# Kernel optimization log

Hardware: AMD Instinct MI355X
Metric: run time of the kernel (lower is better)

## Reference

```python
import jax, jax.numpy as jnp
import numpy as np

N, D_IN, D_P, N_HEADS, N_CTRS, D_OUT = 8192, 256, 64, 8, 128, 256


def setup_inputs() -> dict:
    key = jax.random.key(0)
    k = jax.random.split(key, 6)
    x = jax.random.normal(k[0], (N, D_IN), dtype=jnp.float32)
    ctrs = jax.random.normal(k[1], (N_HEADS, N_CTRS, D_P), dtype=jnp.float32) * 0.5
    Wv = jax.random.normal(k[2], (N_HEADS, N_CTRS, D_P, D_P), dtype=jnp.float32) * 0.02
    Ov = jax.random.normal(k[3], (N_HEADS, N_CTRS, D_P), dtype=jnp.float32) * 0.02
    Wq = jax.random.normal(k[4], (D_IN, D_P, N_HEADS), dtype=jnp.float32) * 0.05
    Wo = jax.random.normal(k[5], (N_HEADS * D_P, D_OUT), dtype=jnp.float32) * 0.02
    return {"x": x, "ctrs": ctrs, "Wv": Wv, "Ov": Ov, "Wq": Wq, "Wo": Wo}


def reference(x, ctrs, Wv, Ov, Wq, Wo):
    # project input per head: (N,d_in) x (d_in,d_p,h) -> (h,N,d_p)
    x_in = jnp.einsum('ni,iph->hnp', x, Wq)
    # RBF soft assignments over centroids: (h,N,c)
    dist_sq = jnp.sum((x_in[:, :, None, :] - ctrs[:, None, :, :]) ** 2, axis=-1)
    assignments = jax.nn.softmax(-dist_sq, axis=2)
    # soft-weighted per-cluster matrices: (h,N,g,p)
    scored_weights = jnp.einsum('hnc,hcgp->hngp', assignments, Wv)
    # soft-weighted offsets: (h,N,p)
    scored_offsets = jnp.einsum('hnc,hcp->hnp', assignments, Ov)
    # elementwise multiply (broadcast over g) then reduce over g, as in original
    heads_out = jnp.sum(scored_weights * x_in[:, :, None, :], axis=2) + scored_offsets
    # NOTE: original reshapes (h,N,p) directly into (N, h*p) in row-major order
    heads_out = heads_out.reshape(x.shape[0], N_HEADS * D_P)
    return heads_out @ Wo
```

## Files before the change

### kernel.cpp

```cpp
#include <hip/hip_runtime.h>
#include <math.h>

#define NROWS 8192
#define DIN   256
#define NH    8
#define NC    128
#define DOUT  256

typedef unsigned short ushort_t;
typedef __attribute__((ext_vector_type(8))) short bf16x8;
typedef __attribute__((ext_vector_type(4))) float f32x4;
typedef __attribute__((ext_vector_type(8))) unsigned short u16x8;

static __device__ __forceinline__ ushort_t f2bf(float f) {
  union { float f; unsigned u; } v; v.f = f;
  unsigned r = v.u + 0x7fffu + ((v.u >> 16) & 1u);
  return (ushort_t)(r >> 16);
}
static __device__ __forceinline__ float bf2f(ushort_t h) {
  union { unsigned u; float f; } v; v.u = ((unsigned)h) << 16;
  return v.f;
}

#define MFMA16(a, b, c) __builtin_amdgcn_mfma_f32_16x16x32_bf16((a), (b), (c), 0, 0, 0)
#define GLOAD_LDS16(g, l)                                                     \
  __builtin_amdgcn_global_load_lds(                                           \
      (const __attribute__((address_space(1))) void*)(g),                     \
      (__attribute__((address_space(3))) void*)(l), 16, 0, 0)

__global__ __launch_bounds__(256) void prep_kernel(
    const float* __restrict__ Wq, const float* __restrict__ ctrs,
    const float* __restrict__ Wo, const float* __restrict__ Wv,
    const float* __restrict__ Ov, ushort_t* __restrict__ wcvtT,
    ushort_t* __restrict__ ctr3T, float* __restrict__ cbias,
    ushort_t* __restrict__ WoT, ushort_t* __restrict__ W2bT) {
  int bid = blockIdx.x;
  int t = threadIdx.x;
  if (bid < 512) {
    int j = bid, k = t;
    int h = j >> 6, p = j & 63;
    float v = Wq[((size_t)k * 64 + p) * 8 + h];
    ushort_t hi = f2bf(v), lo = f2bf(v - bf2f(hi));
    wcvtT[(size_t)j * 512 + k]       = hi;
    wcvtT[(size_t)j * 512 + 256 + k] = lo;
  } else if (bid < 768) {
    int idx = (bid - 512) * 4 + (t >> 6);
    int p = t & 63;
    float v = ctrs[(size_t)idx * 64 + p];
    float sq = v * v;
    #pragma unroll
    for (int off = 32; off >= 1; off >>= 1) sq += __shfl_xor(sq, off, 64);
    if (p == 0) cbias[idx] = -sq;
    ushort_t hi = f2bf(v), lo = f2bf(v - bf2f(hi));
    ctr3T[(size_t)idx * 192 + p]       = hi;
    ctr3T[(size_t)idx * 192 + 64 + p]  = lo;
    ctr3T[(size_t)idx * 192 + 128 + p] = hi;
  } else if (bid < 1280) {
    int k = bid - 768;
    int n = t;
    WoT[(size_t)n * 512 + k] = f2bf(Wo[(size_t)k * 256 + n]);
  } else {
    int b = (bid - 1280) * 4 + (t >> 6);
    int p = t & 63;
    int h = b >> 7, c = b & 127;
    const float* wv = Wv + (size_t)b * 4096;
    float acc = 0.f;
    #pragma unroll 16
    for (int g = 0; g < 64; ++g) acc += wv[g * 64 + p];
    W2bT[((size_t)h * 128 + p) * 128 + c]      = f2bf(acc);
    W2bT[((size_t)h * 128 + 64 + p) * 128 + c] = f2bf(Ov[(size_t)b * 64 + p]);
  }
}

__global__ __launch_bounds__(256) void gemm2_kernel(
    const ushort_t* __restrict__ A, const ushort_t* __restrict__ Bt,
    float* __restrict__ out) {
  __shared__ ushort_t At[32 * 64];
  __shared__ ushort_t Bl[64 * 64];
  const int t = threadIdx.x;
  const int w = t >> 6, l = t & 63;
  const int wr = w >> 1, wc = w & 1;
  const int m0 = (blockIdx.x >> 2) * 32, n0 = (blockIdx.x & 3) * 64;
  const int lr = l & 15, lk = l >> 4;

  f32x4 acc[2];
  #pragma unroll
  for (int b = 0; b < 2; ++b) acc[b] = (f32x4){0.f, 0.f, 0.f, 0.f};

  for (int k0 = 0; k0 < 512; k0 += 64) {
    {
      int q = w * 64 + l;
      int row = q >> 3, s = q & 7;
      int kl = k0 + ((s ^ (row & 7)) << 3);
      GLOAD_LDS16(A + (size_t)(m0 + row) * 512 + kl,
                  (char*)At + (size_t)w * 1024);
    }
    #pragma unroll
    for (int i = 0; i < 2; ++i) {
      int q = (i * 4 + w) * 64 + l;
      int row = q >> 3, s = q & 7;
      int kl = k0 + ((s ^ (row & 7)) << 3);
      GLOAD_LDS16(Bt + (size_t)(n0 + row) * 512 + kl,
                  (char*)Bl + (size_t)(i * 4 + w) * 1024);
    }
    __syncthreads();
    #pragma unroll
    for (int kk = 0; kk < 2; ++kk) {
      int rowa = wr * 16 + lr;
      int sa = (kk * 4 + lk) ^ (rowa & 7);
      bf16x8 af = *(const bf16x8*)((const char*)At + rowa * 128 + sa * 16);
      #pragma unroll
      for (int b = 0; b < 2; ++b) {
        int row = wc * 32 + b * 16 + lr;
        int s = (kk * 4 + lk) ^ (row & 7);
        bf16x8 bfr = *(const bf16x8*)((const char*)Bl + row * 128 + s * 16);
        acc[b] = MFMA16(af, bfr, acc[b]);
      }
    }
    __syncthreads();
  }
  #pragma unroll
  for (int b = 0; b < 2; ++b) {
    #pragma unroll
    for (int r = 0; r < 4; ++r) {
      int rowg = m0 + wr * 16 + lk * 4 + r;
      int colg = n0 + wc * 32 + b * 16 + lr;
      out[(size_t)rowg * 256 + colg] = acc[b][r];
    }
  }
}

__global__ __launch_bounds__(256, 2) void fused_pair_kernel(
    const float* __restrict__ x,
    const ushort_t* __restrict__ wcvtT,
    const ushort_t* __restrict__ ctr3T,
    const float* __restrict__ cbias,
    const ushort_t* __restrict__ W2bT,
    ushort_t* __restrict__ ho2) {
  __shared__ __align__(16) char Au_raw[36864];
  __shared__ char B0lds[16384];
  __shared__ char B1lds[16384];
  __shared__ float cb_lds[128];

  ushort_t* Axh = (ushort_t*)Au_raw;
  ushort_t* Axl = (ushort_t*)(Au_raw + 18432);
  ushort_t* A1  = (ushort_t*)Au_raw;
  ushort_t* A2  = (ushort_t*)Au_raw;

  const int t = threadIdx.x;
  const int w = t >> 6, l = t & 63;
  const int lr = l & 15, lk = l >> 4;
  const int h = blockIdx.x >> 6;
  const int n0 = (blockIdx.x & 63) * 128;

#define STAGE_B(BUF, SRC, LDB, KOFF)                                          \
  {                                                                           \
    _Pragma("unroll")                                                         \
    for (int i = 0; i < 4; ++i) {                                             \
      int q = (i * 4 + w) * 64 + l;                                           \
      int row = q >> 3, s = q & 7;                                            \
      GLOAD_LDS16((SRC) + (size_t)(h * 128 + row) * (LDB) + (KOFF) +          \
                      ((s ^ (row & 7)) << 3),                                 \
                  (char*)(BUF) + (size_t)(i * 4 + w) * 1024);                 \
    }                                                                         \
  }

#define STAGE_BX(BUF, KC)                                                     \
  {                                                                           \
    _Pragma("unroll")                                                         \
    for (int i = 0; i < 4; ++i) {                                             \
      int q = (i * 4 + w) * 64 + l;                                           \
      int row = q >> 3, s = q & 7;                                            \
      int sw = (s ^ (row & 7)) << 3;                                          \
      int jj = h * 64 + (row & 63);                                           \
      int koff = (row < 64 ? 0 : 256) + (KC) * 64 + sw;                       \
      GLOAD_LDS16(wcvtT + (size_t)jj * 512 + koff,                            \
                  (char*)(BUF) + (size_t)(i * 4 + w) * 1024);                 \
    }                                                                         \
  }

#define MFMA_STEP(BUF, ACC0, ACC1, KBASE, ASPLIT)                             \
  {                                                                           \
    _Pragma("unroll")                                                         \
    for (int kk = 0; kk < 2; ++kk) {                                          \
      int klog = (KBASE) + kk * 32 + lk * 8;                                  \
      int kp = (ASPLIT) ? (klog < 64 ? klog : klog - 64) : klog;              \
      bf16x8 af0 = *(const bf16x8*)&A1[(w * 16 + lr) * 136 + kp];             \
      bf16x8 af1 = *(const bf16x8*)&A1[(64 + w * 16 + lr) * 136 + kp];        \
      _Pragma("unroll")                                                       \
      for (int cj = 0; cj < 8; ++cj) {                                        \
        int brow = cj * 16 + lr;                                              \
        int slot = (kk * 4 + lk) ^ (brow & 7);                                \
        bf16x8 bfr =                                                          \
            *(const bf16x8*)((const char*)(BUF) + brow * 128 + slot * 16);    \
        (ACC0)[cj] = MFMA16(af0, bfr, (ACC0)[cj]);                            \
        (ACC1)[cj] = MFMA16(af1, bfr, (ACC1)[cj]);                            \
      }                                                                       \
    }                                                                         \
  }

#define MFMAX(BUF)                                                            \
  {                                                                           \
    _Pragma("unroll")                                                         \
    for (int kk = 0; kk < 2; ++kk) {                                          \
      bf16x8 ah0 = *(const bf16x8*)&Axh[(w * 16 + lr) * 72 + kk * 32 + lk * 8];     \
      bf16x8 al0 = *(const bf16x8*)&Axl[(w * 16 + lr) * 72 + kk * 32 + lk * 8];     \
      bf16x8 ah1 = *(const bf16x8*)&Axh[(64 + w * 16 + lr) * 72 + kk * 32 + lk * 8];\
      bf16x8 al1 = *(const bf16x8*)&Axl[(64 + w * 16 + lr) * 72 + kk * 32 + lk * 8];\
      _Pragma("unroll")                                                       \
      for (int cj = 0; cj < 4; ++cj) {                                        \
        int rh = cj * 16 + lr;                                                \
        int slot = (kk * 4 + lk) ^ (rh & 7);                                  \
        bf16x8 bh = *(const bf16x8*)((const char*)(BUF) + rh * 128 + slot * 16);\
        bf16x8 bl = *(const bf16x8*)((const char*)(BUF) + (64 + rh) * 128 + slot * 16);\
        acc_x0[cj] = MFMA16(ah0, bh, acc_x0[cj]);                             \
        acc_x0[cj] = MFMA16(al0, bh, acc_x0[cj]);                             \
        acc_x0[cj] = MFMA16(ah0, bl, acc_x0[cj]);                             \
        acc_x1[cj] = MFMA16(ah1, bh, acc_x1[cj]);                             \
        acc_x1[cj] = MFMA16(al1, bh, acc_x1[cj]);                             \
        acc_x1[cj] = MFMA16(ah1, bl, acc_x1[cj]);                             \
      }                                                                       \
    }                                                                         \
  }

#define BAR() __builtin_amdgcn_s_barrier()
#define SCHED() __builtin_amdgcn_sched_barrier(0)
#define WAITALL_BAR()                                                         \
  {                                                                           \
    asm volatile("s_waitcnt vmcnt(0) lgkmcnt(0)" ::: "memory");               \
    SCHED(); BAR(); SCHED();                                                  \
  }

  const int xrow = t >> 2;
  const int xseg = (t & 3) << 4;
  const float* xb0 = x + (size_t)(n0 + xrow) * 256 + xseg;
  const float* xb1 = xb0 + 64 * 256;
  float4 xr[8];

#define LOAD_X(KC)                                                            \
  {                                                                           \
    _Pragma("unroll")                                                         \
    for (int j = 0; j < 4; ++j) xr[j]     = *(const float4*)(xb0 + (KC) * 64 + j * 4); \
    _Pragma("unroll")                                                         \
    for (int j = 0; j < 4; ++j) xr[4 + j] = *(const float4*)(xb1 + (KC) * 64 + j * 4); \
  }

#define CVT_AX()                                                              \
  {                                                                           \
    _Pragma("unroll")                                                         \
    for (int hf = 0; hf < 2; ++hf) {                                          \
      u16x8 hv0, hv1, lv0, lv1;                                               \
      _Pragma("unroll")                                                       \
      for (int j = 0; j < 2; ++j) {                                           \
        float f4[8] = {xr[hf*4 + j*2].x, xr[hf*4 + j*2].y, xr[hf*4 + j*2].z,  \
                       xr[hf*4 + j*2].w, xr[hf*4 + j*2 + 1].x,                \
                       xr[hf*4 + j*2 + 1].y, xr[hf*4 + j*2 + 1].z,            \
                       xr[hf*4 + j*2 + 1].w};                                 \
        _Pragma("unroll")                                                     \
        for (int e = 0; e < 8; ++e) {                                         \
          ushort_t hi = f2bf(f4[e]);                                          \
          if (j == 0) { hv0[e] = hi; lv0[e] = f2bf(f4[e] - bf2f(hi)); }       \
          else        { hv1[e] = hi; lv1[e] = f2bf(f4[e] - bf2f(hi)); }       \
        }                                                                     \
      }                                                                       \
      int ro = hf * 64 + xrow;                                                \
      *(u16x8*)&Axh[ro * 72 + xseg]     = hv0;                                \
      *(u16x8*)&Axh[ro * 72 + xseg + 8] = hv1;                                \
      *(u16x8*)&Axl[ro * 72 + xseg]     = lv0;                                \
      *(u16x8*)&Axl[ro * 72 + xseg + 8] = lv1;                                \
    }                                                                         \
  }

#define SOFTMAX(ACC, ROFF)                                                    \
  {                                                                           \
    float cbv[8];                                                             \
    _Pragma("unroll")                                                         \
    for (int cj = 0; cj < 8; ++cj) cbv[cj] = cb_lds[cj * 16 + lr];            \
    _Pragma("unroll")                                                         \
    for (int r = 0; r < 4; ++r) {                                             \
      float v[8];                                                             \
      float m = -1e30f;                                                       \
      _Pragma("unroll")                                                       \
      for (int cj = 0; cj < 8; ++cj) {                                        \
        v[cj] = 2.f * (ACC)[cj][r] + cbv[cj];                                 \
        m = fmaxf(m, v[cj]);                                                  \
      }                                                                       \
      m = fmaxf(m, __shfl_xor(m, 1, 64));                                     \
      m = fmaxf(m, __shfl_xor(m, 2, 64));                                     \
      m = fmaxf(m, __shfl_xor(m, 4, 64));                                     \
      m = fmaxf(m, __shfl_xor(m, 8, 64));                                     \
      float s = 0.f;                                                          \
      _Pragma("unroll")                                                       \
      for (int cj = 0; cj < 8; ++cj) {                                        \
        v[cj] = __expf(v[cj] - m);                                            \
        s += v[cj];                                                           \
      }                                                                       \
      s += __shfl_xor(s, 1, 64);                                              \
      s += __shfl_xor(s, 2, 64);                                              \
      s += __shfl_xor(s, 4, 64);                                              \
      s += __shfl_xor(s, 8, 64);                                              \
      float inv = 1.f / s;                                                    \
      int row = (ROFF) + w * 16 + lk * 4 + r;                                 \
      _Pragma("unroll")                                                       \
      for (int cj = 0; cj < 8; ++cj)                                          \
        A2[row * 136 + cj * 16 + lr] = f2bf(v[cj] * inv);                     \
    }                                                                         \
  }

  cb_lds[t & 127] = cbias[h * 128 + (t & 127)];
  STAGE_BX(B0lds, 0);
  LOAD_X(0);
  f32x4 acc_x0[4], acc_x1[4];
  #pragma unroll
  for (int cj = 0; cj < 4; ++cj) {
    acc_x0[cj] = (f32x4){0.f, 0.f, 0.f, 0.f};
    acc_x1[cj] = (f32x4){0.f, 0.f, 0.f, 0.f};
  }
  CVT_AX();
  WAITALL_BAR();

  STAGE_BX(B1lds, 1);
  LOAD_X(1);
  MFMAX(B0lds);
  CVT_AX();
  WAITALL_BAR();
  STAGE_BX(B0lds, 2);
  LOAD_X(2);
  MFMAX(B1lds);
  CVT_AX();
  WAITALL_BAR();
  STAGE_BX(B1lds, 3);
  LOAD_X(3);
  MFMAX(B0lds);
  CVT_AX();
  WAITALL_BAR();
  STAGE_B(B0lds, ctr3T, 192, 0);
  MFMAX(B1lds);
  WAITALL_BAR();

  STAGE_B(B1lds, ctr3T, 192, 64);
  #pragma unroll
  for (int cj = 0; cj < 4; ++cj) {
    #pragma unroll
    for (int r = 0; r < 4; ++r) {
      int row = w * 16 + lk * 4 + r;
      int p = cj * 16 + lr;
      float v0 = acc_x0[cj][r];
      ushort_t hi0 = f2bf(v0);
      A1[row * 136 + p] = hi0;
      A1[row * 136 + 64 + p] = f2bf(v0 - bf2f(hi0));
      float v1 = acc_x1[cj][r];
      ushort_t hi1 = f2bf(v1);
      A1[(64 + row) * 136 + p] = hi1;
      A1[(64 + row) * 136 + 64 + p] = f2bf(v1 - bf2f(hi1));
    }
  }
  f32x4 acc0[8], acc1[8];
  #pragma unroll
  for (int cj = 0; cj < 8; ++cj) {
    acc0[cj] = (f32x4){0.f, 0.f, 0.f, 0.f};
    acc1[cj] = (f32x4){0.f, 0.f, 0.f, 0.f};
  }
  MFMA_STEP(B0lds, acc0, acc1, 0, 1);
  WAITALL_BAR();
  STAGE_B(B0lds, ctr3T, 192, 128);
  MFMA_STEP(B1lds, acc0, acc1, 64, 1);
  WAITALL_BAR();
  STAGE_B(B1lds, W2bT, 128, 0);
  MFMA_STEP(B0lds, acc0, acc1, 128, 1);
  WAITALL_BAR();
  STAGE_B(B0lds, W2bT, 128, 64);
  SOFTMAX(acc0, 0);
  SOFTMAX(acc1, 64);
  f32x4 accT0[8], accT1[8];
  #pragma unroll
  for (int cj = 0; cj < 8; ++cj) {
    accT0[cj] = (f32x4){0.f, 0.f, 0.f, 0.f};
    accT1[cj] = (f32x4){0.f, 0.f, 0.f, 0.f};
  }
  MFMA_STEP(B1lds, accT0, accT1, 0, 0);
  WAITALL_BAR();
  MFMA_STEP(B0lds, accT0, accT1, 64, 0);
  #pragma unroll
  for (int cj = 0; cj < 4; ++cj) {
    #pragma unroll
    for (int r = 0; r < 4; ++r) {
      int row = w * 16 + lk * 4 + r;
      int p = cj * 16 + lr;
      float hov0 = acc_x0[cj][r] * accT0[cj][r] + accT0[cj + 4][r];
      ((ushort_t*)B1lds)[row * 64 + p] = f2bf(hov0);
      float hov1 = acc_x1[cj][r] * accT1[cj][r] + accT1[cj + 4][r];
      ((ushort_t*)B1lds)[(64 + row) * 64 + p] = f2bf(hov1);
    }
  }
  asm volatile("s_waitcnt lgkmcnt(0)" ::: "memory");
  SCHED(); BAR(); SCHED();
  #pragma unroll
  for (int i = 0; i < 4; ++i) {
    int q = i * 256 + t;
    int row = q >> 3, s = q & 7;
    uint4 v = *(const uint4*)((const char*)B1lds + row * 128 + s * 16);
    *(uint4*)(ho2 + ((size_t)h * NROWS + n0 + row) * 64 + s * 8) = v;
  }
#undef STAGE_B
#undef STAGE_BX
#undef MFMA_STEP
#undef MFMAX
#undef BAR
#undef SCHED
#undef WAITALL_BAR
#undef LOAD_X
#undef CVT_AX
#undef SOFTMAX
}

extern "C" void kernel_launch(void* const* d_in, const int* in_sizes, int n_in,
                              void* d_out, int out_size, void* d_ws, size_t ws_size,
                              hipStream_t stream) {
  (void)in_sizes; (void)n_in; (void)out_size; (void)ws_size;
  const float* x    = (const float*)d_in[0];
  const float* ctrs = (const float*)d_in[1];
  const float* Wv   = (const float*)d_in[2];
  const float* Ov   = (const float*)d_in[3];
  const float* Wq   = (const float*)d_in[4];
  const float* Wo   = (const float*)d_in[5];
  float* out = (float*)d_out;

  char* wsb = (char*)d_ws;
  ushort_t* wcvtT = (ushort_t*)wsb;
  ushort_t* ctr3T = (ushort_t*)(wsb + 524288);
  float*    cb    = (float*)   (wsb + 917504);
  ushort_t* W2bT  = (ushort_t*)(wsb + 921600);
  ushort_t* WoT   = (ushort_t*)(wsb + 1183744);
  ushort_t* ho2   = (ushort_t*)(wsb + 2097152);

  prep_kernel<<<1536, 256, 0, stream>>>(Wq, ctrs, Wo, Wv, Ov,
                                        wcvtT, ctr3T, cb, WoT, W2bT);
  fused_pair_kernel<<<512, 256, 0, stream>>>(x, wcvtT, ctr3T, cb, W2bT, ho2);
  gemm2_kernel<<<1024, 256, 0, stream>>>(ho2, WoT, out);
}
```

Measured before the change: 40.98 us.

## Double-buffer x register loads and use packed bf16 conversion instructions

Splits the x register buffer into two sets so each chunk's global loads are issued one stage earlier, with partial vmcnt waits instead of full drains at each barrier. It also replaces the scalar software bf16 rounding with the packed v_cvt_pk_bf16_f32 instruction for the hi/lo split. This aims to hide global load latency and cut VALU conversion work, at the cost of more registers and reliance on exact vmcnt accounting.

```diff
diff --git a/kernel.cpp b/kernel.cpp
--- a/kernel.cpp
+++ b/kernel.cpp
@@ -20,6 +20,26 @@
 static __device__ __forceinline__ float bf2f(ushort_t h) {
   union { unsigned u; float f; } v; v.u = ((unsigned)h) << 16;
   return v.f;
+}
+static __device__ __forceinline__ float ub2f(unsigned u) {
+  union { unsigned u; float f; } v; v.u = u;
+  return v.f;
+}
+static __device__ __forceinline__ unsigned cvtpk(float a, float b) {
+  unsigned r;
+  asm("v_cvt_pk_bf16_f32 %0, %1, %2" : "=v"(r) : "v"(a), "v"(b));
+  return r;
+}
+static __device__ __forceinline__ void cvt2(const float4 a, const float4 b,
+                                            uint4* H, uint4* L) {
+  unsigned h0 = cvtpk(a.x, a.y), h1 = cvtpk(a.z, a.w);
+  unsigned h2 = cvtpk(b.x, b.y), h3 = cvtpk(b.z, b.w);
+  *H = make_uint4(h0, h1, h2, h3);
+  unsigned l0 = cvtpk(a.x - ub2f(h0 << 16), a.y - ub2f(h0 & 0xffff0000u));
+  unsigned l1 = cvtpk(a.z - ub2f(h1 << 16), a.w - ub2f(h1 & 0xffff0000u));
+  unsigned l2 = cvtpk(b.x - ub2f(h2 << 16), b.y - ub2f(h2 & 0xffff0000u));
+  unsigned l3 = cvtpk(b.z - ub2f(h3 << 16), b.w - ub2f(h3 & 0xffff0000u));
+  *L = make_uint4(l0, l1, l2, l3);
 }
 
 #define MFMA16(a, b, c) __builtin_amdgcn_mfma_f32_16x16x32_bf16((a), (b), (c), 0, 0, 0)
@@ -230,44 +250,50 @@
     asm volatile("s_waitcnt vmcnt(0) lgkmcnt(0)" ::: "memory");               \
     SCHED(); BAR(); SCHED();                                                  \
   }
+#define WAIT8_BAR()                                                           \
+  {                                                                           \
+    asm volatile("s_waitcnt vmcnt(8) lgkmcnt(0)" ::: "memory");               \
+    SCHED(); BAR(); SCHED();                                                  \
+  }
+#define LGKM_BAR()                                                            \
+  {                                                                           \
+    asm volatile("s_waitcnt lgkmcnt(0)" ::: "memory");                        \
+    SCHED(); BAR(); SCHED();                                                  \
+  }
 
   const int xrow = t >> 2;
   const int xseg = (t & 3) << 4;
   const float* xb0 = x + (size_t)(n0 + xrow) * 256 + xseg;
   const float* xb1 = xb0 + 64 * 256;
-  float4 xr[8];
-
-#define LOAD_X(KC)                                                            \
-  {                                                                           \
-    _Pragma("unroll")                                                         \
-    for (int j = 0; j < 4; ++j) xr[j]     = *(const float4*)(xb0 + (KC) * 64 + j * 4); \
-    _Pragma("unroll")                                                         \
-    for (int j = 0; j < 4; ++j) xr[4 + j] = *(const float4*)(xb1 + (KC) * 64 + j * 4); \
-  }
-
-#define CVT_AX()                                                              \
+  float4 xra[8], xrb[8];
+
+#define LOAD_XA(KC)                                                           \
+  {                                                                           \
+    _Pragma("unroll")                                                         \
+    for (int j = 0; j < 4; ++j) xra[j]     = *(const float4*)(xb0 + (KC) * 64 + j * 4); \
+    _Pragma("unroll")                                                         \
+    for (int j = 0; j < 4; ++j) xra[4 + j] = *(const float4*)(xb1 + (KC) * 64 + j * 4); \
+  }
+#define LOAD_XB(KC)                                                           \
+  {                                                                           \
+    _Pragma("unroll")                                                         \
+    for (int j = 0; j < 4; ++j) xrb[j]     = *(const float4*)(xb0 + (KC) * 64 + j * 4); \
+    _Pragma("unroll")                                                         \
+    for (int j = 0; j < 4; ++j) xrb[4 + j] = *(const float4*)(xb1 + (KC) * 64 + j * 4); \
+  }
+
+#define CVT_AX(SET)                                                           \
   {                                                                           \
     _Pragma("unroll")                                                         \
     for (int hf = 0; hf < 2; ++hf) {                                          \
-      u16x8 hv0, hv1, lv0, lv1;                                               \
-      _Pragma("unroll")                                                       \
-      for (int j = 0; j < 2; ++j) {                                           \
-        float f4[8] = {xr[hf*4 + j*2].x, xr[hf*4 + j*2].y, xr[hf*4 + j*2].z,  \
-                       xr[hf*4 + j*2].w, xr[hf*4 + j*2 + 1].x,                \
-                       xr[hf*4 + j*2 + 1].y, xr[hf*4 + j*2 + 1].z,            \
-                       xr[hf*4 + j*2 + 1].w};                                 \
-        _Pragma("unroll")                                                     \
-        for (int e = 0; e < 8; ++e) {                                         \
-          ushort_t hi = f2bf(f4[e]);                                          \
-          if (j == 0) { hv0[e] = hi; lv0[e] = f2bf(f4[e] - bf2f(hi)); }       \
-          else        { hv1[e] = hi; lv1[e] = f2bf(f4[e] - bf2f(hi)); }       \
-        }                                                                     \
-      }                                                                       \
+      uint4 H0, L0, H1, L1;                                                   \
+      cvt2(SET[hf * 4 + 0], SET[hf * 4 + 1], &H0, &L0);                       \
+      cvt2(SET[hf * 4 + 2], SET[hf * 4 + 3], &H1, &L1);                       \
       int ro = hf * 64 + xrow;                                                \
-      *(u16x8*)&Axh[ro * 72 + xseg]     = hv0;                                \
-      *(u16x8*)&Axh[ro * 72 + xseg + 8] = hv1;                                \
-      *(u16x8*)&Axl[ro * 72 + xseg]     = lv0;                                \
-      *(u16x8*)&Axl[ro * 72 + xseg + 8] = lv1;                                \
+      *(uint4*)&Axh[ro * 72 + xseg]     = H0;                                 \
+      *(uint4*)&Axh[ro * 72 + xseg + 8] = H1;                                 \
+      *(uint4*)&Axl[ro * 72 + xseg]     = L0;                                 \
+      *(uint4*)&Axl[ro * 72 + xseg + 8] = L1;                                 \
     }                                                                         \
   }
 
@@ -309,30 +335,38 @@
 
   cb_lds[t & 127] = cbias[h * 128 + (t & 127)];
   STAGE_BX(B0lds, 0);
-  LOAD_X(0);
+  SCHED();
+  LOAD_XA(0);
+  SCHED();
+  LOAD_XB(1);
+  SCHED();
   f32x4 acc_x0[4], acc_x1[4];
   #pragma unroll
   for (int cj = 0; cj < 4; ++cj) {
     acc_x0[cj] = (f32x4){0.f, 0.f, 0.f, 0.f};
     acc_x1[cj] = (f32x4){0.f, 0.f, 0.f, 0.f};
   }
-  CVT_AX();
-  WAITALL_BAR();
+  CVT_AX(xra);
+  LGKM_BAR();
 
   STAGE_BX(B1lds, 1);
-  LOAD_X(1);
+  SCHED();
+  LOAD_XA(2);
+  SCHED();
   MFMAX(B0lds);
-  CVT_AX();
-  WAITALL_BAR();
+  CVT_AX(xrb);
+  WAIT8_BAR();
   STAGE_BX(B0lds, 2);
-  LOAD_X(2);
+  SCHED();
+  LOAD_XB(3);
+  SCHED();
   MFMAX(B1lds);
-  CVT_AX();
-  WAITALL_BAR();
+  CVT_AX(xra);
+  WAIT8_BAR();
   STAGE_BX(B1lds, 3);
-  LOAD_X(3);
+  SCHED();
   MFMAX(B0lds);
-  CVT_AX();
+  CVT_AX(xrb);
   WAITALL_BAR();
   STAGE_B(B0lds, ctr3T, 192, 0);
   MFMAX(B1lds);
@@ -409,7 +443,10 @@
 #undef BAR
 #undef SCHED
 #undef WAITALL_BAR
-#undef LOAD_X
+#undef WAIT8_BAR
+#undef LGKM_BAR
+#undef LOAD_XA
+#undef LOAD_XB
 #undef CVT_AX
 #undef SOFTMAX
 }
```

Measured after the change: 41.39 us. No clear change (+1.0%).

## Use 512 threads per block in fused kernel, one 16-row tile per wave

Applied to the files above, without the earlier changes.

The fused projection/softmax/assignment kernel now launches 512 threads (8 waves) per block instead of 256, and each wave handles a single 16-row slice rather than two. Per-thread accumulators, x loads and staging loops are halved, which lowers register pressure and allows a higher occupancy hint (launch bounds 512,4). The trade-off is that each B tile staged in LDS is reused across fewer MFMAs per wave, and more waves must meet at each barrier.

```diff
diff --git a/kernel.cpp b/kernel.cpp
--- a/kernel.cpp
+++ b/kernel.cpp
@@ -130,7 +130,7 @@
   }
 }
 
-__global__ __launch_bounds__(256, 2) void fused_pair_kernel(
+__global__ __launch_bounds__(512, 4) void fused_pair_kernel(
     const float* __restrict__ x,
     const ushort_t* __restrict__ wcvtT,
     const ushort_t* __restrict__ ctr3T,
@@ -156,45 +156,43 @@
 #define STAGE_B(BUF, SRC, LDB, KOFF)                                          \
   {                                                                           \
     _Pragma("unroll")                                                         \
-    for (int i = 0; i < 4; ++i) {                                             \
-      int q = (i * 4 + w) * 64 + l;                                           \
+    for (int i = 0; i < 2; ++i) {                                             \
+      int q = (i * 8 + w) * 64 + l;                                           \
       int row = q >> 3, s = q & 7;                                            \
       GLOAD_LDS16((SRC) + (size_t)(h * 128 + row) * (LDB) + (KOFF) +          \
                       ((s ^ (row & 7)) << 3),                                 \
-                  (char*)(BUF) + (size_t)(i * 4 + w) * 1024);                 \
+                  (char*)(BUF) + (size_t)(i * 8 + w) * 1024);                 \
     }                                                                         \
   }
 
 #define STAGE_BX(BUF, KC)                                                     \
   {                                                                           \
     _Pragma("unroll")                                                         \
-    for (int i = 0; i < 4; ++i) {                                             \
-      int q = (i * 4 + w) * 64 + l;                                           \
+    for (int i = 0; i < 2; ++i) {                                             \
+      int q = (i * 8 + w) * 64 + l;                                           \
       int row = q >> 3, s = q & 7;                                            \
       int sw = (s ^ (row & 7)) << 3;                                          \
       int jj = h * 64 + (row & 63);                                           \
       int koff = (row < 64 ? 0 : 256) + (KC) * 64 + sw;                       \
       GLOAD_LDS16(wcvtT + (size_t)jj * 512 + koff,                            \
-                  (char*)(BUF) + (size_t)(i * 4 + w) * 1024);                 \
-    }                                                                         \
-  }
-
-#define MFMA_STEP(BUF, ACC0, ACC1, KBASE, ASPLIT)                             \
+                  (char*)(BUF) + (size_t)(i * 8 + w) * 1024);                 \
+    }                                                                         \
+  }
+
+#define MFMA_STEP(BUF, ACC, KBASE, ASPLIT)                                    \
   {                                                                           \
     _Pragma("unroll")                                                         \
     for (int kk = 0; kk < 2; ++kk) {                                          \
       int klog = (KBASE) + kk * 32 + lk * 8;                                  \
       int kp = (ASPLIT) ? (klog < 64 ? klog : klog - 64) : klog;              \
-      bf16x8 af0 = *(const bf16x8*)&A1[(w * 16 + lr) * 136 + kp];             \
-      bf16x8 af1 = *(const bf16x8*)&A1[(64 + w * 16 + lr) * 136 + kp];        \
+      bf16x8 af = *(const bf16x8*)&A1[(w * 16 + lr) * 136 + kp];              \
       _Pragma("unroll")                                                       \
       for (int cj = 0; cj < 8; ++cj) {                                        \
         int brow = cj * 16 + lr;                                              \
         int slot = (kk * 4 + lk) ^ (brow & 7);                                \
         bf16x8 bfr =                                                          \
             *(const bf16x8*)((const char*)(BUF) + brow * 128 + slot * 16);    \
-        (ACC0)[cj] = MFMA16(af0, bfr, (ACC0)[cj]);                            \
-        (ACC1)[cj] = MFMA16(af1, bfr, (ACC1)[cj]);                            \
+        (ACC)[cj] = MFMA16(af, bfr, (ACC)[cj]);                               \
       }                                                                       \
     }                                                                         \
   }
@@ -203,22 +201,17 @@
   {                                                                           \
     _Pragma("unroll")                                                         \
     for (int kk = 0; kk < 2; ++kk) {                                          \
-      bf16x8 ah0 = *(const bf16x8*)&Axh[(w * 16 + lr) * 72 + kk * 32 + lk * 8];     \
-      bf16x8 al0 = *(const bf16x8*)&Axl[(w * 16 + lr) * 72 + kk * 32 + lk * 8];     \
-      bf16x8 ah1 = *(const bf16x8*)&Axh[(64 + w * 16 + lr) * 72 + kk * 32 + lk * 8];\
-      bf16x8 al1 = *(const bf16x8*)&Axl[(64 + w * 16 + lr) * 72 + kk * 32 + lk * 8];\
+      bf16x8 ah = *(const bf16x8*)&Axh[(w * 16 + lr) * 72 + kk * 32 + lk * 8];\
+      bf16x8 al = *(const bf16x8*)&Axl[(w * 16 + lr) * 72 + kk * 32 + lk * 8];\
       _Pragma("unroll")                                                       \
       for (int cj = 0; cj < 4; ++cj) {                                        \
         int rh = cj * 16 + lr;                                                \
         int slot = (kk * 4 + lk) ^ (rh & 7);                                  \
         bf16x8 bh = *(const bf16x8*)((const char*)(BUF) + rh * 128 + slot * 16);\
         bf16x8 bl = *(const bf16x8*)((const char*)(BUF) + (64 + rh) * 128 + slot * 16);\
-        acc_x0[cj] = MFMA16(ah0, bh, acc_x0[cj]);                             \
-        acc_x0[cj] = MFMA16(al0, bh, acc_x0[cj]);                             \
-        acc_x0[cj] = MFMA16(ah0, bl, acc_x0[cj]);                             \
-        acc_x1[cj] = MFMA16(ah1, bh, acc_x1[cj]);                             \
-        acc_x1[cj] = MFMA16(al1, bh, acc_x1[cj]);                             \
-        acc_x1[cj] = MFMA16(ah1, bl, acc_x1[cj]);                             \
+        acc_x[cj] = MFMA16(ah, bh, acc_x[cj]);                                \
+        acc_x[cj] = MFMA16(al, bh, acc_x[cj]);                                \
+        acc_x[cj] = MFMA16(ah, bl, acc_x[cj]);                                \
       }                                                                       \
     }                                                                         \
   }
@@ -233,45 +226,36 @@
 
   const int xrow = t >> 2;
   const int xseg = (t & 3) << 4;
-  const float* xb0 = x + (size_t)(n0 + xrow) * 256 + xseg;
-  const float* xb1 = xb0 + 64 * 256;
-  float4 xr[8];
+  const float* xb = x + (size_t)(n0 + xrow) * 256 + xseg;
+  float4 xr[4];
 
 #define LOAD_X(KC)                                                            \
   {                                                                           \
     _Pragma("unroll")                                                         \
-    for (int j = 0; j < 4; ++j) xr[j]     = *(const float4*)(xb0 + (KC) * 64 + j * 4); \
-    _Pragma("unroll")                                                         \
-    for (int j = 0; j < 4; ++j) xr[4 + j] = *(const float4*)(xb1 + (KC) * 64 + j * 4); \
+    for (int j = 0; j < 4; ++j) xr[j] = *(const float4*)(xb + (KC) * 64 + j * 4); \
   }
 
 #define CVT_AX()                                                              \
   {                                                                           \
-    _Pragma("unroll")                                                         \
-    for (int hf = 0; hf < 2; ++hf) {                                          \
-      u16x8 hv0, hv1, lv0, lv1;                                               \
-      _Pragma("unroll")                                                       \
-      for (int j = 0; j < 2; ++j) {                                           \
-        float f4[8] = {xr[hf*4 + j*2].x, xr[hf*4 + j*2].y, xr[hf*4 + j*2].z,  \
-                       xr[hf*4 + j*2].w, xr[hf*4 + j*2 + 1].x,                \
-                       xr[hf*4 + j*2 + 1].y, xr[hf*4 + j*2 + 1].z,            \
-                       xr[hf*4 + j*2 + 1].w};                                 \
-        _Pragma("unroll")                                                     \
-        for (int e = 0; e < 8; ++e) {                                         \
-          ushort_t hi = f2bf(f4[e]);                                          \
-          if (j == 0) { hv0[e] = hi; lv0[e] = f2bf(f4[e] - bf2f(hi)); }       \
-          else        { hv1[e] = hi; lv1[e] = f2bf(f4[e] - bf2f(hi)); }       \
-        }                                                                     \
+    u16x8 hv0, hv1, lv0, lv1;                                                 \
+    _Pragma("unroll")                                                         \
+    for (int j = 0; j < 2; ++j) {                                             \
+      float f4[8] = {xr[j*2].x, xr[j*2].y, xr[j*2].z, xr[j*2].w,              \
+                     xr[j*2+1].x, xr[j*2+1].y, xr[j*2+1].z, xr[j*2+1].w};     \
+      _Pragma("unroll")                                                       \
+      for (int e = 0; e < 8; ++e) {                                           \
+        ushort_t hi = f2bf(f4[e]);                                            \
+        if (j == 0) { hv0[e] = hi; lv0[e] = f2bf(f4[e] - bf2f(hi)); }         \
+        else        { hv1[e] = hi; lv1[e] = f2bf(f4[e] - bf2f(hi)); }         \
       }                                                                       \
-      int ro = hf * 64 + xrow;                                                \
-      *(u16x8*)&Axh[ro * 72 + xseg]     = hv0;                                \
-      *(u16x8*)&Axh[ro * 72 + xseg + 8] = hv1;                                \
-      *(u16x8*)&Axl[ro * 72 + xseg]     = lv0;                                \
-      *(u16x8*)&Axl[ro * 72 + xseg + 8] = lv1;                                \
-    }                                                                         \
-  }
-
-#define SOFTMAX(ACC, ROFF)                                                    \
+    }                                                                         \
+    *(u16x8*)&Axh[xrow * 72 + xseg]     = hv0;                                \
+    *(u16x8*)&Axh[xrow * 72 + xseg + 8] = hv1;                                \
+    *(u16x8*)&Axl[xrow * 72 + xseg]     = lv0;                                \
+    *(u16x8*)&Axl[xrow * 72 + xseg + 8] = lv1;                                \
+  }
+
+#define SOFTMAX(ACC)                                                          \
   {                                                                           \
     float cbv[8];                                                             \
     _Pragma("unroll")                                                         \
@@ -300,7 +284,7 @@
       s += __shfl_xor(s, 4, 64);                                              \
       s += __shfl_xor(s, 8, 64);                                              \
       float inv = 1.f / s;                                                    \
-      int row = (ROFF) + w * 16 + lk * 4 + r;                                 \
+      int row = w * 16 + lk * 4 + r;                                          \
       _Pragma("unroll")                                                       \
       for (int cj = 0; cj < 8; ++cj)                                          \
         A2[row * 136 + cj * 16 + lr] = f2bf(v[cj] * inv);                     \
@@ -310,12 +294,9 @@
   cb_lds[t & 127] = cbias[h * 128 + (t & 127)];
   STAGE_BX(B0lds, 0);
   LOAD_X(0);
-  f32x4 acc_x0[4], acc_x1[4];
-  #pragma unroll
-  for (int cj = 0; cj < 4; ++cj) {
-    acc_x0[cj] = (f32x4){0.f, 0.f, 0.f, 0.f};
-    acc_x1[cj] = (f32x4){0.f, 0.f, 0.f, 0.f};
-  }
+  f32x4 acc_x[4];
+  #pragma unroll
+  for (int cj = 0; cj < 4; ++cj) acc_x[cj] = (f32x4){0.f, 0.f, 0.f, 0.f};
   CVT_AX();
   WAITALL_BAR();
 
@@ -345,59 +326,46 @@
     for (int r = 0; r < 4; ++r) {
       int row = w * 16 + lk * 4 + r;
       int p = cj * 16 + lr;
-      float v0 = acc_x0[cj][r];
+      float v0 = acc_x[cj][r];
       ushort_t hi0 = f2bf(v0);
       A1[row * 136 + p] = hi0;
       A1[row * 136 + 64 + p] = f2bf(v0 - bf2f(hi0));
-      float v1 = acc_x1[cj][r];
-      ushort_t hi1 = f2bf(v1);
-      A1[(64 + row) * 136 + p] = hi1;
-      A1[(64 + row) * 136 + 64 + p] = f2bf(v1 - bf2f(hi1));
-    }
-  }
-  f32x4 acc0[8], acc1[8];
-  #pragma unroll
-  for (int cj = 0; cj < 8; ++cj) {
-    acc0[cj] = (f32x4){0.f, 0.f, 0.f, 0.f};
-    acc1[cj] = (f32x4){0.f, 0.f, 0.f, 0.f};
-  }
-  MFMA_STEP(B0lds, acc0, acc1, 0, 1);
+    }
+  }
+  f32x4 acc[8];
+  #pragma unroll
+  for (int cj = 0; cj < 8; ++cj) acc[cj] = (f32x4){0.f, 0.f, 0.f, 0.f};
+  MFMA_STEP(B0lds, acc, 0, 1);
   WAITALL_BAR();
   STAGE_B(B0lds, ctr3T, 192, 128);
-  MFMA_STEP(B1lds, acc0, acc1, 64, 1);
+  MFMA_STEP(B1lds, acc, 64, 1);
   WAITALL_BAR();
   STAGE_B(B1lds, W2bT, 128, 0);
-  MFMA_STEP(B0lds, acc0, acc1, 128, 1);
+  MFMA_STEP(B0lds, acc, 128, 1);
   WAITALL_BAR();
   STAGE_B(B0lds, W2bT, 128, 64);
-  SOFTMAX(acc0, 0);
-  SOFTMAX(acc1, 64);
-  f32x4 accT0[8], accT1[8];
-  #pragma unroll
-  for (int cj = 0; cj < 8; ++cj) {
-    accT0[cj] = (f32x4){0.f, 0.f, 0.f, 0.f};
-    accT1[cj] = (f32x4){0.f, 0.f, 0.f, 0.f};
-  }
-  MFMA_STEP(B1lds, accT0, accT1, 0, 0);
-  WAITALL_BAR();
-  MFMA_STEP(B0lds, accT0, accT1, 64, 0);
+  SOFTMAX(acc);
+  f32x4 accT[8];
+  #pragma unroll
+  for (int cj = 0; cj < 8; ++cj) accT[cj] = (f32x4){0.f, 0.f, 0.f, 0.f};
+  MFMA_STEP(B1lds, accT, 0, 0);
+  WAITALL_BAR();
+  MFMA_STEP(B0lds, accT, 64, 0);
   #pragma unroll
   for (int cj = 0; cj < 4; ++cj) {
     #pragma unroll
     for (int r = 0; r < 4; ++r) {
       int row = w * 16 + lk * 4 + r;
       int p = cj * 16 + lr;
-      float hov0 = acc_x0[cj][r] * accT0[cj][r] + accT0[cj + 4][r];
-      ((ushort_t*)B1lds)[row * 64 + p] = f2bf(hov0);
-      float hov1 = acc_x1[cj][r] * accT1[cj][r] + accT1[cj + 4][r];
-      ((ushort_t*)B1lds)[(64 + row) * 64 + p] = f2bf(hov1);
+      float hov = acc_x[cj][r] * accT[cj][r] + accT[cj + 4][r];
+      ((ushort_t*)B1lds)[row * 64 + p] = f2bf(hov);
     }
   }
   asm volatile("s_waitcnt lgkmcnt(0)" ::: "memory");
   SCHED(); BAR(); SCHED();
   #pragma unroll
-  for (int i = 0; i < 4; ++i) {
-    int q = i * 256 + t;
+  for (int i = 0; i < 2; ++i) {
+    int q = i * 512 + t;
     int row = q >> 3, s = q & 7;
     uint4 v = *(const uint4*)((const char*)B1lds + row * 128 + s * 16);
     *(uint4*)(ho2 + ((size_t)h * NROWS + n0 + row) * 64 + s * 8) = v;
@@ -436,6 +404,6 @@
 
   prep_kernel<<<1536, 256, 0, stream>>>(Wq, ctrs, Wo, Wv, Ov,
                                         wcvtT, ctr3T, cb, WoT, W2bT);
-  fused_pair_kernel<<<512, 256, 0, stream>>>(x, wcvtT, ctr3T, cb, W2bT, ho2);
+  fused_pair_kernel<<<512, 512, 0, stream>>>(x, wcvtT, ctr3T, cb, W2bT, ho2);
   gemm2_kernel<<<1024, 256, 0, stream>>>(ho2, WoT, out);
 }
```

Result: faster. 39.86 us (-2.7%).
